# Optimization experiments

Hardware: AMD Instinct MI355X
Metric: run time of the kernel (lower is better)

## Reference

```python
import jax, jax.numpy as jnp
import numpy as np

# Dims: batch N, in_channels C (>=75 so the 0.25/0.75 channel weighting is active),
# prototypes O, 3x3 kernel, 56x56 feature map.
N, C, H, W = 32, 150, 56, 56
O = 225
KH = KW = 3
K = KH * KW
D = C * K  # unfolded feature dim = 1350
SPLIT = 75  # weight_cdist: channels [:75] weight 0.25, [75:] weight 0.75


def setup_inputs() -> dict:
    key = jax.random.key(0)
    k1, k2 = jax.random.split(key)
    x = jax.random.uniform(k1, (N, C, H, W), dtype=jnp.float32)
    # kaiming_uniform_ on a (O, D) matrix: bound = sqrt(6 / fan_in), fan_in = D
    bound = float(np.sqrt(6.0 / D))
    weight = jax.random.uniform(k2, (O, D), jnp.float32, -bound, bound)
    return {"x": x, "weight": weight}


def reference(x, weight):
    n = x.shape[0]
    # im2col, channel-major feature ordering (c, kh, kw) -- matches torch F.unfold
    patches = jax.lax.conv_general_dilated_patches(
        x, (KH, KW), (1, 1), ((1, 1), (1, 1)))  # (N, C*K, H, W)
    windows = patches.reshape(n, D, H * W).transpose(0, 2, 1)  # (N, L, D)
    # per-channel weights, repeated over the K kernel positions
    w = jnp.where(jnp.arange(C) < SPLIT, 0.25, 0.75).astype(x.dtype)
    wfull = jnp.repeat(w, K)  # (D,)
    # weighted squared distance: sum_d wfull_d * (x_d - p_d)^2
    #   = ||x||_w^2 + ||p||_w^2 - 2 * x . (w * p)   (GEMM form, no NxOxLxD tensor)
    x2 = jnp.einsum('nld,d->nl', windows * windows, wfull)          # (N, L)
    p2 = jnp.einsum('od,d->o', weight * weight, wfull)              # (O,)
    xp = jnp.einsum('nld,od->nlo', windows, weight * wfull)         # (N, L, O)
    d2 = x2[:, :, None] + p2[None, None, :] - 2.0 * xp
    dist = jnp.sqrt(jnp.maximum(d2, 1e-12))  # clamp tiny negative GEMM round-off
    # (N, L, O) -> (N, O, H, W)
    return dist.transpose(0, 2, 1).reshape(n, O, H, W)
```

## Files before the change

kernel.cpp:

```cpp
#include <hip/hip_runtime.h>

#define N_B   32
#define C_IN  150
#define HH    56
#define WW    56
#define O_P   225
#define D_F   1350
#define SPLIT 75

#define C_PAD 160
#define O_PAD 256
#define PSTR  176
#define NPLANE 58

#define SW    2540.0f
#define SC_I  (1.0f / 322580.0f)

typedef __attribute__((ext_vector_type(4))) int int4v;
typedef __attribute__((ext_vector_type(16))) int i32x16;
typedef unsigned char u8;
typedef unsigned int uint_t;

#define XT_OFF 0
#define WT_OFF 16056320
#define AO_OFF (WT_OFF + 368640)
#define SQ_OFF (AO_OFF + 1024)

#define TIDX(c, w) ((c) * 57 + ((c) >> 4) + (w))

__global__ __launch_bounds__(256) void prep_x(const float* __restrict__ x,
                                              u8* __restrict__ xt,
                                              float* __restrict__ sq) {
  __shared__ float tile[150 * 57 + 9 + 56 + 1];
  __shared__ float sp[4][WW];
  const int n = blockIdx.y, h = blockIdx.x, tid = threadIdx.x;

  for (int idx = tid; idx < C_IN * 14; idx += 256) {
    int c = idx / 14, w4 = (idx % 14) * 4;
    const float4 v = *(const float4*)(&x[((size_t)(n * C_IN + c) * HH + h) * WW + w4]);
    tile[TIDX(c, w4 + 0)] = v.x;
    tile[TIDX(c, w4 + 1)] = v.y;
    tile[TIDX(c, w4 + 2)] = v.z;
    tile[TIDX(c, w4 + 3)] = v.w;
  }
  __syncthreads();

  uint4* xt128 = (uint4*)(xt + (size_t)((n * HH + h) * WW) * C_PAD);
  for (int idx = tid; idx < WW * (C_PAD / 16); idx += 256) {
    int w = idx / (C_PAD / 16), q = idx % (C_PAD / 16), c0 = q * 16;
    uint_t words[4];
#pragma unroll
    for (int wd = 0; wd < 4; ++wd) {
      uint_t a = 0;
#pragma unroll
      for (int b = 0; b < 4; ++b) {
        int c = c0 + wd * 4 + b;
        int v = -127;
        if (c < C_IN) v = __float2int_rn(tile[TIDX(c, w)] * 254.f) - 127;
        a |= ((uint_t)(u8)(char)v) << (8 * b);
      }
      words[wd] = a;
    }
    xt128[idx] = make_uint4(words[0], words[1], words[2], words[3]);
  }

  if (tid < 224) {
    int w = tid >> 2, p = tid & 3;
    int cb = p * 38, ce = min(cb + 38, C_IN);
    float s = 0.f;
    for (int c = cb; c < ce; ++c) {
      float v = tile[TIDX(c, w)];
      s += ((c < SPLIT) ? 0.25f : 0.75f) * v * v;
    }
    sp[p][w] = s;
  }
  __syncthreads();
  if (tid < WW)
    sq[(n * HH + h) * WW + tid] = sp[0][tid] + sp[1][tid] + sp[2][tid] + sp[3][tid];
}

__global__ __launch_bounds__(256) void prep_w(const float* __restrict__ wgt,
                                              u8* __restrict__ wt,
                                              float* __restrict__ ao) {
  const int o = blockIdx.x, tid = threadIdx.x;
  const int ot = o >> 5, ol = o & 31;

  for (int idx = tid; idx < 9 * C_PAD; idx += 256) {
    int t = idx / C_PAD, c = idx % C_PAD;
    int v = 0;
    if (o < O_P && c < C_IN) {
      float wc = (c < SPLIT) ? 0.25f : 0.75f;
      float f = wgt[o * D_F + c * 9 + t] * wc * SW;
      v = __float2int_rn(fminf(fmaxf(f, -127.f), 127.f));
    }
    int kc = c >> 5, hi2 = (c >> 4) & 1, b = c & 15;
    wt[((((size_t)(t * 8 + ot) * 5 + kc) * 2 + hi2) * 32 + ol) * 16 + b] = (u8)(char)v;
  }

  float s1 = 0.f, s2 = 0.f;
  if (o < O_P)
    for (int d = tid; d < D_F; d += 256) {
      int c = d / 9;
      float wc = (c < SPLIT) ? 0.25f : 0.75f;
      float f = wgt[o * D_F + d] * wc * SW;
      float wq = (float)__float2int_rn(fminf(fmaxf(f, -127.f), 127.f));
      s1 += wq;
      s2 += wq * wq / wc;
    }
  __shared__ float r1[256], r2[256];
  r1[tid] = s1; r2[tid] = s2;
  __syncthreads();
  for (int off = 128; off > 0; off >>= 1) {
    if (tid < off) { r1[tid] += r1[tid + off]; r2[tid] += r2[tid + off]; }
    __syncthreads();
  }
  if (tid == 0) ao[o] = r2[0] / (SW * SW) - r1[0] / SW;
}

__global__ __launch_bounds__(256, 3) void sfm_main(
    const u8* __restrict__ xt, const u8* __restrict__ wt,
    const float* __restrict__ aog, const float* __restrict__ sqg,
    float* __restrict__ out) {
  __shared__ __align__(16) u8 xtile[3 * NPLANE * PSTR];
  __shared__ float aos[O_PAD];
  __shared__ float sqs[3][NPLANE];
  __shared__ float x2row[64];

  const int bid0 = blockIdx.y * 56 + blockIdx.x;
  const int bid = (bid0 & 7) * ((N_B * HH) >> 3) + (bid0 >> 3);
  const int h0 = bid % HH, n = bid / HH;
  const int tid = threadIdx.x, lane = tid & 63, wv = tid >> 6;
  const int l31 = lane & 31, hi = lane >> 5;

  for (int idx = tid; idx < 3 * WW * (C_PAD / 16); idx += 256) {
    int dh = idx / (WW * 10), rem = idx % (WW * 10);
    int w = rem / 10, q = rem % 10;
    int hh = h0 + dh - 1;
    uint4 v = make_uint4(0x81818181u, 0x81818181u, 0x81818181u, 0x81818181u);
    if (hh >= 0 && hh < HH)
      v = *(const uint4*)(xt + ((size_t)((n * HH + hh) * WW + w) * C_PAD + q * 16));
    *(uint4*)(&xtile[(dh * NPLANE + (w + 1)) * PSTR + q * 16]) = v;
  }
  for (int idx = tid; idx < 60; idx += 256) {
    int dh = idx / 20, r = idx % 20, side = r / 10, q = r % 10;
    int pos = side ? 57 : 0;
    *(uint4*)(&xtile[(dh * NPLANE + pos) * PSTR + q * 16]) =
        make_uint4(0x81818181u, 0x81818181u, 0x81818181u, 0x81818181u);
  }
  for (int idx = tid; idx < 3 * NPLANE; idx += 256) {
    int dh = idx / NPLANE, col = idx % NPLANE;
    int hh = h0 + dh - 1, w = col - 1;
    float v = 0.f;
    if (hh >= 0 && hh < HH && w >= 0 && w < WW) v = sqg[(n * HH + hh) * WW + w];
    sqs[dh][col] = v;
  }
  aos[tid] = (tid < O_P) ? aog[tid] : 0.f;
  __syncthreads();

  if (tid < 64) {
    float s = 0.f;
    if (tid < WW) {
#pragma unroll
      for (int a = 0; a < 3; ++a)
        s += sqs[a][tid] + sqs[a][tid + 1] + sqs[a][tid + 2];
    }
    x2row[tid] = s;
  }
  __syncthreads();

  int vb[2][3];
#pragma unroll
  for (int i = 0; i < 2; ++i)
#pragma unroll
    for (int d = 0; d < 3; ++d)
      vb[i][d] = min(i * 32 + l31 + d, 57) * PSTR + hi * 16;

  const u8* ap0 = wt + ((size_t)(wv * 2 + 0) * 5120 + hi * 512 + l31 * 16);
  const u8* ap1 = wt + ((size_t)(wv * 2 + 1) * 5120 + hi * 512 + l31 * 16);

  const i32x16 z = {0, 0, 0, 0, 0, 0, 0, 0, 0, 0, 0, 0, 0, 0, 0, 0};
  i32x16 acc[2][2] = {{z, z}, {z, z}};

#pragma unroll
  for (int t = 0; t < 9; ++t) {
    const int dh = t / 3, dwo = t % 3;
    const u8* a0 = ap0 + t * 40960;
    const u8* a1 = ap1 + t * 40960;
    const u8* b0 = &xtile[dh * (NPLANE * PSTR) + vb[0][dwo]];
    const u8* b1 = &xtile[dh * (NPLANE * PSTR) + vb[1][dwo]];
#pragma unroll
    for (int kc = 0; kc < 5; ++kc) {
      int4v af0 = *(const int4v*)(a0 + kc * 1024);
      int4v af1 = *(const int4v*)(a1 + kc * 1024);
      int4v bf0 = *(const int4v*)(b0 + kc * 32);
      int4v bf1 = *(const int4v*)(b1 + kc * 32);
      acc[0][0] = __builtin_amdgcn_mfma_i32_32x32x32_i8(af0, bf0, acc[0][0], 0, 0, 0);
      acc[1][0] = __builtin_amdgcn_mfma_i32_32x32x32_i8(af1, bf0, acc[1][0], 0, 0, 0);
      acc[0][1] = __builtin_amdgcn_mfma_i32_32x32x32_i8(af0, bf1, acc[0][1], 0, 0, 0);
      acc[1][1] = __builtin_amdgcn_mfma_i32_32x32x32_i8(af1, bf1, acc[1][1], 0, 0, 0);
    }
  }

#pragma unroll
  for (int jo = 0; jo < 2; ++jo) {
    const int ob = wv * 64 + jo * 32 + hi * 4;
#pragma unroll
    for (int ip = 0; ip < 2; ++ip) {
      const int w = ip * 32 + l31;
      if (w < WW) {
        const float x2v = x2row[w];
#pragma unroll
        for (int rg = 0; rg < 16; ++rg) {
          const int o = ob + (rg & 3) + 8 * (rg >> 2);
          if (o < O_P) {
            float d2 = x2v + aos[o] - SC_I * (float)acc[jo][ip][rg];
            out[((size_t)(n * O_P + o) * HH + h0) * WW + w] = sqrtf(fmaxf(d2, 1e-12f));
          }
        }
      }
    }
  }
}

extern "C" void kernel_launch(void* const* d_in, const int* in_sizes, int n_in,
                              void* d_out, int out_size, void* d_ws, size_t ws_size,
                              hipStream_t stream) {
  const float* x      = (const float*)d_in[0];
  const float* weight = (const float*)d_in[1];
  float* out = (float*)d_out;
  char* ws = (char*)d_ws;

  u8* xt = (u8*)(ws + XT_OFF);
  u8* wt = (u8*)(ws + WT_OFF);
  float* ao = (float*)(ws + AO_OFF);
  float* sq = (float*)(ws + SQ_OFF);

  prep_x<<<dim3(HH, N_B), 256, 0, stream>>>(x, xt, sq);
  prep_w<<<dim3(O_PAD), 256, 0, stream>>>(weight, wt, ao);
  sfm_main<<<dim3(HH, N_B), 256, 0, stream>>>(xt, wt, ao, sq, out);
}
```

Baseline: 213.2 us.

## Process two output rows per block with register-prefetched fragments and reordered weights

Each main-kernel block now computes two consecutive output rows from a four-plane LDS tile, so adjacent row halos are shared and the grid is halved. The weight layout is reordered so that each wave's A fragments sit contiguously per step, and the MFMA loop is flattened into 45 steps that load the next A/B fragments into registers while the current MFMAs run. The fourth input plane is fetched into registers early and written to LDS after the first row's compute. The x2 window sum is now read directly from global memory. The cost is more registers, fewer blocks, and one extra sync point between the two rows.

After: 521.0 us. 144% more time.

```diff
diff --git a/kernel.cpp b/kernel.cpp
--- a/kernel.cpp
+++ b/kernel.cpp
@@ -12,6 +12,7 @@
 #define O_PAD 256
 #define PSTR  176
 #define NPLANE 58
+#define PLSZ  (NPLANE * PSTR)
 
 #define SW    2540.0f
 #define SC_I  (1.0f / 322580.0f)
@@ -83,7 +84,7 @@
                                               u8* __restrict__ wt,
                                               float* __restrict__ ao) {
   const int o = blockIdx.x, tid = threadIdx.x;
-  const int ot = o >> 5, ol = o & 31;
+  const int wv2 = o >> 6, j2 = (o >> 5) & 1, ol = o & 31;
 
   for (int idx = tid; idx < 9 * C_PAD; idx += 256) {
     int t = idx / C_PAD, c = idx % C_PAD;
@@ -94,7 +95,8 @@
       v = __float2int_rn(fminf(fmaxf(f, -127.f), 127.f));
     }
     int kc = c >> 5, hi2 = (c >> 4) & 1, b = c & 15;
-    wt[((((size_t)(t * 8 + ot) * 5 + kc) * 2 + hi2) * 32 + ol) * 16 + b] = (u8)(char)v;
+    wt[(size_t)wv2 * 92160 + (t * 5 + kc) * 2048 + j2 * 1024 + hi2 * 512 + ol * 16 + b] =
+        (u8)(char)v;
   }
 
   float s1 = 0.f, s2 = 0.f;
@@ -105,7 +107,7 @@
       float f = wgt[o * D_F + d] * wc * SW;
       float wq = (float)__float2int_rn(fminf(fmaxf(f, -127.f), 127.f));
       s1 += wq;
-      s2 += wq * wq / wc;
+      s2 += wq * wq * ((c < SPLIT) ? 4.0f : (4.0f / 3.0f));
     }
   __shared__ float r1[256], r2[256];
   r1[tid] = s1; r2[tid] = s2;
@@ -121,104 +123,136 @@
     const u8* __restrict__ xt, const u8* __restrict__ wt,
     const float* __restrict__ aog, const float* __restrict__ sqg,
     float* __restrict__ out) {
-  __shared__ __align__(16) u8 xtile[3 * NPLANE * PSTR];
+  __shared__ __align__(16) u8 xtile[4 * PLSZ];
   __shared__ float aos[O_PAD];
-  __shared__ float sqs[3][NPLANE];
-  __shared__ float x2row[64];
-
-  const int bid0 = blockIdx.y * 56 + blockIdx.x;
-  const int bid = (bid0 & 7) * ((N_B * HH) >> 3) + (bid0 >> 3);
-  const int h0 = bid % HH, n = bid / HH;
+  __shared__ float x2row[2][64];
+
+  const int bid0 = blockIdx.y * 28 + blockIdx.x;
+  const int bid = (bid0 & 7) * 112 + (bid0 >> 3);
+  const int n = bid / 28, h0 = (bid % 28) * 2;
   const int tid = threadIdx.x, lane = tid & 63, wv = tid >> 6;
   const int l31 = lane & 31, hi = lane >> 5;
 
-  for (int idx = tid; idx < 3 * WW * (C_PAD / 16); idx += 256) {
+  for (int idx = tid; idx < 3 * WW * 10; idx += 256) {
     int dh = idx / (WW * 10), rem = idx % (WW * 10);
     int w = rem / 10, q = rem % 10;
     int hh = h0 + dh - 1;
     uint4 v = make_uint4(0x81818181u, 0x81818181u, 0x81818181u, 0x81818181u);
     if (hh >= 0 && hh < HH)
       v = *(const uint4*)(xt + ((size_t)((n * HH + hh) * WW + w) * C_PAD + q * 16));
-    *(uint4*)(&xtile[(dh * NPLANE + (w + 1)) * PSTR + q * 16]) = v;
-  }
-  for (int idx = tid; idx < 60; idx += 256) {
+    *(uint4*)(&xtile[(size_t)dh * PLSZ + (w + 1) * PSTR + q * 16]) = v;
+  }
+  for (int idx = tid; idx < 80; idx += 256) {
     int dh = idx / 20, r = idx % 20, side = r / 10, q = r % 10;
     int pos = side ? 57 : 0;
-    *(uint4*)(&xtile[(dh * NPLANE + pos) * PSTR + q * 16]) =
+    *(uint4*)(&xtile[(size_t)dh * PLSZ + pos * PSTR + q * 16]) =
         make_uint4(0x81818181u, 0x81818181u, 0x81818181u, 0x81818181u);
   }
-  for (int idx = tid; idx < 3 * NPLANE; idx += 256) {
-    int dh = idx / NPLANE, col = idx % NPLANE;
-    int hh = h0 + dh - 1, w = col - 1;
-    float v = 0.f;
-    if (hh >= 0 && hh < HH && w >= 0 && w < WW) v = sqg[(n * HH + hh) * WW + w];
-    sqs[dh][col] = v;
+  if (tid < 128) {
+    int r = tid >> 6, w = tid & 63;
+    float s = 0.f;
+    if (w < WW) {
+#pragma unroll
+      for (int a = 0; a < 3; ++a) {
+        int hh = h0 + r + a - 1;
+        if (hh >= 0 && hh < HH) {
+#pragma unroll
+          for (int b = 0; b < 3; ++b) {
+            int ww2 = w + b - 1;
+            if (ww2 >= 0 && ww2 < WW) s += sqg[(n * HH + hh) * WW + ww2];
+          }
+        }
+      }
+    }
+    x2row[r][w] = s;
   }
   aos[tid] = (tid < O_P) ? aog[tid] : 0.f;
   __syncthreads();
 
-  if (tid < 64) {
-    float s = 0.f;
-    if (tid < WW) {
-#pragma unroll
-      for (int a = 0; a < 3; ++a)
-        s += sqs[a][tid] + sqs[a][tid + 1] + sqs[a][tid + 2];
-    }
-    x2row[tid] = s;
-  }
-  __syncthreads();
-
-  int vb[2][3];
+  uint4 pl3[3];
+  const int hh3 = h0 + 2;
+#pragma unroll
+  for (int k = 0; k < 3; ++k) {
+    int idx = tid + 256 * k;
+    uint4 v = make_uint4(0x81818181u, 0x81818181u, 0x81818181u, 0x81818181u);
+    if (idx < WW * 10 && hh3 < HH) {
+      int w = idx / 10, q = idx % 10;
+      v = *(const uint4*)(xt + ((size_t)((n * HH + hh3) * WW + w) * C_PAD + q * 16));
+    }
+    pl3[k] = v;
+  }
+
+  const u8* bvp[2][3];
 #pragma unroll
   for (int i = 0; i < 2; ++i)
 #pragma unroll
     for (int d = 0; d < 3; ++d)
-      vb[i][d] = min(i * 32 + l31 + d, 57) * PSTR + hi * 16;
-
-  const u8* ap0 = wt + ((size_t)(wv * 2 + 0) * 5120 + hi * 512 + l31 * 16);
-  const u8* ap1 = wt + ((size_t)(wv * 2 + 1) * 5120 + hi * 512 + l31 * 16);
+      bvp[i][d] = &xtile[min(i * 32 + l31 + d, 57) * PSTR + hi * 16];
+
+  const u8* abase = wt + (size_t)__builtin_amdgcn_readfirstlane(wv) * 92160 +
+                    hi * 512 + l31 * 16;
 
   const i32x16 z = {0, 0, 0, 0, 0, 0, 0, 0, 0, 0, 0, 0, 0, 0, 0, 0};
-  i32x16 acc[2][2] = {{z, z}, {z, z}};
-
-#pragma unroll
-  for (int t = 0; t < 9; ++t) {
-    const int dh = t / 3, dwo = t % 3;
-    const u8* a0 = ap0 + t * 40960;
-    const u8* a1 = ap1 + t * 40960;
-    const u8* b0 = &xtile[dh * (NPLANE * PSTR) + vb[0][dwo]];
-    const u8* b1 = &xtile[dh * (NPLANE * PSTR) + vb[1][dwo]];
-#pragma unroll
-    for (int kc = 0; kc < 5; ++kc) {
-      int4v af0 = *(const int4v*)(a0 + kc * 1024);
-      int4v af1 = *(const int4v*)(a1 + kc * 1024);
-      int4v bf0 = *(const int4v*)(b0 + kc * 32);
-      int4v bf1 = *(const int4v*)(b1 + kc * 32);
+
+  for (int r = 0; r < 2; ++r) {
+    i32x16 acc[2][2] = {{z, z}, {z, z}};
+
+    int4v af0 = *(const int4v*)(abase + 0 * 2048 + 0);
+    int4v af1 = *(const int4v*)(abase + 0 * 2048 + 1024);
+    int4v bf0 = *(const int4v*)(bvp[0][0] + r * PLSZ);
+    int4v bf1 = *(const int4v*)(bvp[1][0] + r * PLSZ);
+
+#pragma unroll
+    for (int s = 0; s < 45; ++s) {
+      int4v an0, an1, bn0, bn1;
+      if (s < 44) {
+        const int s1 = s + 1, t = s1 / 5, kc = s1 % 5;
+        const int dh = t / 3, dwo = t % 3;
+        an0 = *(const int4v*)(abase + s1 * 2048 + 0);
+        an1 = *(const int4v*)(abase + s1 * 2048 + 1024);
+        bn0 = *(const int4v*)(bvp[0][dwo] + (r + dh) * PLSZ + kc * 32);
+        bn1 = *(const int4v*)(bvp[1][dwo] + (r + dh) * PLSZ + kc * 32);
+      }
       acc[0][0] = __builtin_amdgcn_mfma_i32_32x32x32_i8(af0, bf0, acc[0][0], 0, 0, 0);
       acc[1][0] = __builtin_amdgcn_mfma_i32_32x32x32_i8(af1, bf0, acc[1][0], 0, 0, 0);
       acc[0][1] = __builtin_amdgcn_mfma_i32_32x32x32_i8(af0, bf1, acc[0][1], 0, 0, 0);
       acc[1][1] = __builtin_amdgcn_mfma_i32_32x32x32_i8(af1, bf1, acc[1][1], 0, 0, 0);
-    }
-  }
-
-#pragma unroll
-  for (int jo = 0; jo < 2; ++jo) {
-    const int ob = wv * 64 + jo * 32 + hi * 4;
-#pragma unroll
-    for (int ip = 0; ip < 2; ++ip) {
-      const int w = ip * 32 + l31;
-      if (w < WW) {
-        const float x2v = x2row[w];
-#pragma unroll
-        for (int rg = 0; rg < 16; ++rg) {
-          const int o = ob + (rg & 3) + 8 * (rg >> 2);
-          if (o < O_P) {
-            float d2 = x2v + aos[o] - SC_I * (float)acc[jo][ip][rg];
-            out[((size_t)(n * O_P + o) * HH + h0) * WW + w] = sqrtf(fmaxf(d2, 1e-12f));
+      if (s < 44) { af0 = an0; af1 = an1; bf0 = bn0; bf1 = bn1; }
+    }
+
+    if (r == 0) {
+#pragma unroll
+      for (int k = 0; k < 3; ++k) {
+        int idx = tid + 256 * k;
+        if (idx < WW * 10) {
+          int w = idx / 10, q = idx % 10;
+          *(uint4*)(&xtile[(size_t)3 * PLSZ + (w + 1) * PSTR + q * 16]) = pl3[k];
+        }
+      }
+    }
+
+#pragma unroll
+    for (int jo = 0; jo < 2; ++jo) {
+      const int ob = wv * 64 + jo * 32 + hi * 4;
+#pragma unroll
+      for (int ip = 0; ip < 2; ++ip) {
+        const int w = ip * 32 + l31;
+        if (w < WW) {
+          const float x2v = x2row[r][w];
+#pragma unroll
+          for (int rg = 0; rg < 16; ++rg) {
+            const int o = ob + (rg & 3) + 8 * (rg >> 2);
+            if (o < O_P) {
+              float d2 = x2v + aos[o] - SC_I * (float)acc[jo][ip][rg];
+              out[((size_t)(n * O_P + o) * HH + (h0 + r)) * WW + w] =
+                  sqrtf(fmaxf(d2, 1e-12f));
+            }
           }
         }
       }
     }
+
+    if (r == 0) __syncthreads();
   }
 }
 
@@ -237,5 +271,5 @@
 
   prep_x<<<dim3(HH, N_B), 256, 0, stream>>>(x, xt, sq);
   prep_w<<<dim3(O_PAD), 256, 0, stream>>>(weight, wt, ao);
-  sfm_main<<<dim3(HH, N_B), 256, 0, stream>>>(xt, wt, ao, sq, out);
-}
+  sfm_main<<<dim3(28, N_B), 256, 0, stream>>>(xt, wt, ao, sq, out);
+}
```

## Split output-channel work across 8 waves per block with 512 threads

Applied to the files above, without the earlier changes.

The main kernel moves from 4 waves each computing 64 output prototypes to 8 waves each computing 32, so every wave holds two accumulators instead of four. The weight buffer layout is rearranged so each wave reads a contiguous 32-prototype slice. The aim is lower register pressure and more waves in flight to hide LDS and global load latency. The cost is that each wave reloads the shared x tile fragments for fewer MFMAs, raising the ratio of LDS reads to compute. A division in prep_w is also replaced by a multiply.

Result: faster. 204.7 us (-4.0%).

```diff
diff --git a/kernel.cpp b/kernel.cpp
--- a/kernel.cpp
+++ b/kernel.cpp
@@ -12,6 +12,7 @@
 #define O_PAD 256
 #define PSTR  176
 #define NPLANE 58
+#define PLSZ  (NPLANE * PSTR)
 
 #define SW    2540.0f
 #define SC_I  (1.0f / 322580.0f)
@@ -83,7 +84,7 @@
                                               u8* __restrict__ wt,
                                               float* __restrict__ ao) {
   const int o = blockIdx.x, tid = threadIdx.x;
-  const int ot = o >> 5, ol = o & 31;
+  const int wv2 = o >> 6, j2 = (o >> 5) & 1, ol = o & 31;
 
   for (int idx = tid; idx < 9 * C_PAD; idx += 256) {
     int t = idx / C_PAD, c = idx % C_PAD;
@@ -94,7 +95,8 @@
       v = __float2int_rn(fminf(fmaxf(f, -127.f), 127.f));
     }
     int kc = c >> 5, hi2 = (c >> 4) & 1, b = c & 15;
-    wt[((((size_t)(t * 8 + ot) * 5 + kc) * 2 + hi2) * 32 + ol) * 16 + b] = (u8)(char)v;
+    wt[(size_t)wv2 * 92160 + (t * 5 + kc) * 2048 + j2 * 1024 + hi2 * 512 + ol * 16 + b] =
+        (u8)(char)v;
   }
 
   float s1 = 0.f, s2 = 0.f;
@@ -105,7 +107,7 @@
       float f = wgt[o * D_F + d] * wc * SW;
       float wq = (float)__float2int_rn(fminf(fmaxf(f, -127.f), 127.f));
       s1 += wq;
-      s2 += wq * wq / wc;
+      s2 += wq * wq * ((c < SPLIT) ? 4.0f : (4.0f / 3.0f));
     }
   __shared__ float r1[256], r2[256];
   r1[tid] = s1; r2[tid] = s2;
@@ -117,44 +119,44 @@
   if (tid == 0) ao[o] = r2[0] / (SW * SW) - r1[0] / SW;
 }
 
-__global__ __launch_bounds__(256, 3) void sfm_main(
+__global__ __launch_bounds__(512, 4) void sfm_main(
     const u8* __restrict__ xt, const u8* __restrict__ wt,
     const float* __restrict__ aog, const float* __restrict__ sqg,
     float* __restrict__ out) {
-  __shared__ __align__(16) u8 xtile[3 * NPLANE * PSTR];
+  __shared__ __align__(16) u8 xtile[3 * PLSZ];
   __shared__ float aos[O_PAD];
   __shared__ float sqs[3][NPLANE];
   __shared__ float x2row[64];
 
   const int bid0 = blockIdx.y * 56 + blockIdx.x;
-  const int bid = (bid0 & 7) * ((N_B * HH) >> 3) + (bid0 >> 3);
+  const int bid = (bid0 & 7) * 224 + (bid0 >> 3);
   const int h0 = bid % HH, n = bid / HH;
   const int tid = threadIdx.x, lane = tid & 63, wv = tid >> 6;
   const int l31 = lane & 31, hi = lane >> 5;
 
-  for (int idx = tid; idx < 3 * WW * (C_PAD / 16); idx += 256) {
+  for (int idx = tid; idx < 3 * WW * 10; idx += 512) {
     int dh = idx / (WW * 10), rem = idx % (WW * 10);
     int w = rem / 10, q = rem % 10;
     int hh = h0 + dh - 1;
     uint4 v = make_uint4(0x81818181u, 0x81818181u, 0x81818181u, 0x81818181u);
     if (hh >= 0 && hh < HH)
       v = *(const uint4*)(xt + ((size_t)((n * HH + hh) * WW + w) * C_PAD + q * 16));
-    *(uint4*)(&xtile[(dh * NPLANE + (w + 1)) * PSTR + q * 16]) = v;
-  }
-  for (int idx = tid; idx < 60; idx += 256) {
+    *(uint4*)(&xtile[(size_t)dh * PLSZ + (w + 1) * PSTR + q * 16]) = v;
+  }
+  for (int idx = tid; idx < 60; idx += 512) {
     int dh = idx / 20, r = idx % 20, side = r / 10, q = r % 10;
     int pos = side ? 57 : 0;
-    *(uint4*)(&xtile[(dh * NPLANE + pos) * PSTR + q * 16]) =
+    *(uint4*)(&xtile[(size_t)dh * PLSZ + pos * PSTR + q * 16]) =
         make_uint4(0x81818181u, 0x81818181u, 0x81818181u, 0x81818181u);
   }
-  for (int idx = tid; idx < 3 * NPLANE; idx += 256) {
+  for (int idx = tid; idx < 3 * NPLANE; idx += 512) {
     int dh = idx / NPLANE, col = idx % NPLANE;
     int hh = h0 + dh - 1, w = col - 1;
     float v = 0.f;
     if (hh >= 0 && hh < HH && w >= 0 && w < WW) v = sqg[(n * HH + hh) * WW + w];
     sqs[dh][col] = v;
   }
-  aos[tid] = (tid < O_P) ? aog[tid] : 0.f;
+  if (tid < O_PAD) aos[tid] = (tid < O_P) ? aog[tid] : 0.f;
   __syncthreads();
 
   if (tid < 64) {
@@ -175,47 +177,41 @@
     for (int d = 0; d < 3; ++d)
       vb[i][d] = min(i * 32 + l31 + d, 57) * PSTR + hi * 16;
 
-  const u8* ap0 = wt + ((size_t)(wv * 2 + 0) * 5120 + hi * 512 + l31 * 16);
-  const u8* ap1 = wt + ((size_t)(wv * 2 + 1) * 5120 + hi * 512 + l31 * 16);
+  const int wvs = __builtin_amdgcn_readfirstlane(wv);
+  const u8* abase = wt + (size_t)(wvs >> 1) * 92160 + (wvs & 1) * 1024 +
+                    hi * 512 + l31 * 16;
 
   const i32x16 z = {0, 0, 0, 0, 0, 0, 0, 0, 0, 0, 0, 0, 0, 0, 0, 0};
-  i32x16 acc[2][2] = {{z, z}, {z, z}};
+  i32x16 acc[2] = {z, z};
 
 #pragma unroll
   for (int t = 0; t < 9; ++t) {
     const int dh = t / 3, dwo = t % 3;
-    const u8* a0 = ap0 + t * 40960;
-    const u8* a1 = ap1 + t * 40960;
-    const u8* b0 = &xtile[dh * (NPLANE * PSTR) + vb[0][dwo]];
-    const u8* b1 = &xtile[dh * (NPLANE * PSTR) + vb[1][dwo]];
+    const u8* a0 = abase + t * 10240;
+    const u8* b0 = &xtile[dh * PLSZ + vb[0][dwo]];
+    const u8* b1 = &xtile[dh * PLSZ + vb[1][dwo]];
 #pragma unroll
     for (int kc = 0; kc < 5; ++kc) {
-      int4v af0 = *(const int4v*)(a0 + kc * 1024);
-      int4v af1 = *(const int4v*)(a1 + kc * 1024);
+      int4v af  = *(const int4v*)(a0 + kc * 2048);
       int4v bf0 = *(const int4v*)(b0 + kc * 32);
       int4v bf1 = *(const int4v*)(b1 + kc * 32);
-      acc[0][0] = __builtin_amdgcn_mfma_i32_32x32x32_i8(af0, bf0, acc[0][0], 0, 0, 0);
-      acc[1][0] = __builtin_amdgcn_mfma_i32_32x32x32_i8(af1, bf0, acc[1][0], 0, 0, 0);
-      acc[0][1] = __builtin_amdgcn_mfma_i32_32x32x32_i8(af0, bf1, acc[0][1], 0, 0, 0);
-      acc[1][1] = __builtin_amdgcn_mfma_i32_32x32x32_i8(af1, bf1, acc[1][1], 0, 0, 0);
-    }
-  }
-
-#pragma unroll
-  for (int jo = 0; jo < 2; ++jo) {
-    const int ob = wv * 64 + jo * 32 + hi * 4;
-#pragma unroll
-    for (int ip = 0; ip < 2; ++ip) {
-      const int w = ip * 32 + l31;
-      if (w < WW) {
-        const float x2v = x2row[w];
-#pragma unroll
-        for (int rg = 0; rg < 16; ++rg) {
-          const int o = ob + (rg & 3) + 8 * (rg >> 2);
-          if (o < O_P) {
-            float d2 = x2v + aos[o] - SC_I * (float)acc[jo][ip][rg];
-            out[((size_t)(n * O_P + o) * HH + h0) * WW + w] = sqrtf(fmaxf(d2, 1e-12f));
-          }
+      acc[0] = __builtin_amdgcn_mfma_i32_32x32x32_i8(af, bf0, acc[0], 0, 0, 0);
+      acc[1] = __builtin_amdgcn_mfma_i32_32x32x32_i8(af, bf1, acc[1], 0, 0, 0);
+    }
+  }
+
+  const int ob = wv * 32 + hi * 4;
+#pragma unroll
+  for (int ip = 0; ip < 2; ++ip) {
+    const int w = ip * 32 + l31;
+    if (w < WW) {
+      const float x2v = x2row[w];
+#pragma unroll
+      for (int rg = 0; rg < 16; ++rg) {
+        const int o = ob + (rg & 3) + 8 * (rg >> 2);
+        if (o < O_P) {
+          float d2 = x2v + aos[o] - SC_I * (float)acc[ip][rg];
+          out[((size_t)(n * O_P + o) * HH + h0) * WW + w] = sqrtf(fmaxf(d2, 1e-12f));
         }
       }
     }
@@ -237,5 +233,5 @@
 
   prep_x<<<dim3(HH, N_B), 256, 0, stream>>>(x, xt, sq);
   prep_w<<<dim3(O_PAD), 256, 0, stream>>>(weight, wt, ao);
-  sfm_main<<<dim3(HH, N_B), 256, 0, stream>>>(xt, wt, ao, sq, out);
-}
+  sfm_main<<<dim3(56, N_B), 512, 0, stream>>>(xt, wt, ao, sq, out);
+}
```
